# Performance work log

Measured on AMD Instinct MI355X. Metric: run time of the kernel, lower is better.

Reference implementation:

```python
import jax, jax.numpy as jnp
import numpy as np

B, S, D = 1, 2048, 2048
HQ, HKV = 32, 8
HD = D // HQ            # 64
G = HQ // HKV           # 4 query heads per kv head


def setup_inputs() -> dict:
    key = jax.random.key(0)
    ks = jax.random.split(key, 5)
    x = jax.random.normal(ks[0], (B, S, D), jnp.float32)
    # RoPE tables (theta = 10000), shape [S, HD//2]
    inv_freq = 1.0 / (10000.0 ** (np.arange(0, HD, 2, dtype=np.float64) / HD))
    angles = np.outer(np.arange(S, dtype=np.float64), inv_freq)
    freqs_cos = jnp.asarray(np.cos(angles), jnp.float32)
    freqs_sin = jnp.asarray(np.sin(angles), jnp.float32)
    # additive causal mask [1,1,S,S]: 0 on/below diagonal, large negative above
    i = jnp.arange(S)
    causal_mask = jnp.where(i[None, :] <= i[:, None], 0.0, -1e9).astype(jnp.float32)[None, None]
    sc = 1.0 / np.sqrt(D)
    Wq = jax.random.normal(ks[1], (D, HQ * HD), jnp.float32) * sc
    Wk = jax.random.normal(ks[2], (D, HKV * HD), jnp.float32) * sc
    Wv = jax.random.normal(ks[3], (D, HKV * HD), jnp.float32) * sc
    Wo = jax.random.normal(ks[4], (D, D), jnp.float32) * sc
    return {"x": x, "freqs_cos": freqs_cos, "freqs_sin": freqs_sin,
            "causal_mask": causal_mask, "Wq": Wq, "Wk": Wk, "Wv": Wv, "Wo": Wo}


def _rope(t, cos, sin):
    # t: [B,S,H,HD]; complex multiply on interleaved (even, odd) pairs
    b, s, h, d = t.shape
    t2 = t.reshape(b, s, h, d // 2, 2)
    t0, t1 = t2[..., 0], t2[..., 1]
    c = cos[None, :, None, :]
    sn = sin[None, :, None, :]
    out = jnp.stack([t0 * c - t1 * sn, t0 * sn + t1 * c], axis=-1)
    return out.reshape(b, s, h, d)


def reference(x, freqs_cos, freqs_sin, causal_mask, Wq, Wk, Wv, Wo):
    b, s, _ = x.shape
    q = (x @ Wq).reshape(b, s, HQ, HD)
    k = (x @ Wk).reshape(b, s, HKV, HD)
    v = (x @ Wv).reshape(b, s, HKV, HD)
    q = _rope(q, freqs_cos, freqs_sin)
    k = _rope(k, freqs_cos, freqs_sin)
    # GQA without materializing repeat_kv: group query heads per kv head
    q = q.transpose(0, 2, 1, 3).reshape(b, HKV, G, s, HD)   # [b,kv,g,s,d]
    k = k.transpose(0, 2, 1, 3)                              # [b,kv,s,d]
    v = v.transpose(0, 2, 1, 3)                              # [b,kv,s,d]
    scores = jnp.einsum('bkgsd,bktd->bkgst', q, k) / jnp.sqrt(jnp.float32(HD))
    scores = scores + causal_mask[:, :, None]                # [1,1,1,S,S] broadcast
    probs = jax.nn.softmax(scores, axis=-1)
    out = jnp.einsum('bkgst,bktd->bkgsd', probs, v)          # [b,kv,g,s,d]
    out = out.transpose(0, 3, 1, 2, 4).reshape(b, s, D)      # merge heads in (kv,g) order
    return out @ Wo
```

## Files before the change

### kernel.cpp

```cpp
#include <hip/hip_runtime.h>

#define SEQ 2048
#define DMODEL 2048

typedef __attribute__((ext_vector_type(8))) _Float16 half8;
typedef __attribute__((ext_vector_type(4))) float f32x4;
typedef __attribute__((ext_vector_type(16))) float f32x16;

typedef const __attribute__((address_space(1))) void* gptr_t;
typedef __attribute__((address_space(3))) void* lptr_t;

static __device__ __forceinline__ void gload16(const void* g, void* l) {
  __builtin_amdgcn_global_load_lds((gptr_t)g, (lptr_t)l, 16, 0, 0);
}

static __device__ __forceinline__ unsigned short f2h(float f) {
  _Float16 h = (_Float16)f;
  union { _Float16 h; unsigned short u; } v; v.h = h;
  return v.u;
}

static __device__ __forceinline__ unsigned int pkh2(float a, float b) {
  union { __fp16 __attribute__((ext_vector_type(2))) h; unsigned int u; } v;
  v.h = __builtin_amdgcn_cvt_pkrtz(a, b);
  return v.u;
}

__global__ void k_cvt(const float* __restrict__ in, unsigned short* __restrict__ out, int n) {
  int i = (blockIdx.x * 256 + threadIdx.x) * 4;
  if (i >= n) return;
  float4 v = *(const float4*)(in + i);
  ushort4 o;
  o.x = f2h(v.x); o.y = f2h(v.y); o.z = f2h(v.z); o.w = f2h(v.w);
  *(ushort4*)(out + i) = o;
}

__global__ void k_tcvt(const float* __restrict__ in, unsigned short* __restrict__ out,
                       int K, int N, int ldin) {
  __shared__ float tile[32][33];
  int n0 = blockIdx.x * 32, k0 = blockIdx.y * 32;
  int tx = threadIdx.x, ty = threadIdx.y;
  #pragma unroll
  for (int j = ty; j < 32; j += 8)
    tile[j][tx] = in[(long)(k0 + j) * ldin + n0 + tx];
  __syncthreads();
  #pragma unroll
  for (int j = ty; j < 32; j += 8)
    out[(long)(n0 + j) * K + k0 + tx] = f2h(tile[tx][j]);
}

__global__ void k_tvp(const unsigned short* __restrict__ in, unsigned short* __restrict__ out) {
  __shared__ unsigned short tile[32][33];
  int c0 = blockIdx.x * 32, s0 = blockIdx.y * 32;
  int tx = threadIdx.x, ty = threadIdx.y;
  #pragma unroll
  for (int j = ty; j < 32; j += 8)
    tile[j][tx] = in[(long)(s0 + j) * 512 + c0 + tx];
  __syncthreads();
  #pragma unroll
  for (int j = ty; j < 32; j += 8) {
    int c = c0 + j;
    int s = s0 + tx;
    int sp = (s & ~12) | ((s & 8) >> 1) | ((s & 4) << 1);
    out[((long)(c >> 6) * 64 + (c & 63)) * SEQ + sp] = tile[tx][j];
  }
}

static __device__ __forceinline__ void gemm_core(const unsigned short* __restrict__ A,
                                                 const unsigned short* __restrict__ B,
                                                 int K, unsigned short* As, unsigned short* Bs,
                                                 long m0, long n0, int t, int wm, int wn,
                                                 int lr, int lh, f32x4 acc[2][4]) {
  int swc = ((t & 3) ^ ((t >> 3) & 3)) * 8;
  const unsigned short* Ag = A + (m0 + (t >> 2)) * K + swc;
  const unsigned short* Bg = B + (n0 + (t >> 2)) * K + swc;
  #pragma unroll
  for (int i = 0; i < 2; i++)
    #pragma unroll
    for (int j = 0; j < 4; j++)
      acc[i][j] = (f32x4){0.f, 0.f, 0.f, 0.f};

#define STAGE(buf, k0) do { \
    gload16(Ag + (k0), As + (buf) * 4096 + t * 8); \
    gload16(Bg + (k0), Bs + (buf) * 4096 + t * 8); \
  } while (0)

  int T = K >> 5;
  STAGE(0, 0);
  STAGE(1, 32);
  asm volatile("s_waitcnt vmcnt(2)" ::: "memory");
  __builtin_amdgcn_s_barrier();

  int bi = 0;
  for (int ti = 0; ti < T; ti++) {
    if (ti + 2 < T) STAGE((bi + 2) % 3, (ti + 2) * 32);
    const unsigned short* Ab = As + bi * 4096;
    const unsigned short* Bb = Bs + bi * 4096;
    half8 a[2], b[4];
    #pragma unroll
    for (int mf = 0; mf < 2; mf++) {
      int ra = wm * 32 + mf * 16 + lr;
      a[mf] = *(const half8*)&Ab[ra * 32 + ((lh ^ ((ra >> 1) & 3)) * 8)];
    }
    #pragma unroll
    for (int nf = 0; nf < 4; nf++) {
      int rb = wn * 64 + nf * 16 + lr;
      b[nf] = *(const half8*)&Bb[rb * 32 + ((lh ^ ((rb >> 1) & 3)) * 8)];
    }
    #pragma unroll
    for (int mf = 0; mf < 2; mf++)
      #pragma unroll
      for (int nf = 0; nf < 4; nf++)
        acc[mf][nf] = __builtin_amdgcn_mfma_f32_16x16x32_f16(a[mf], b[nf], acc[mf][nf], 0, 0, 0);
    if (ti + 2 < T) asm volatile("s_waitcnt vmcnt(2)" ::: "memory");
    else            asm volatile("s_waitcnt vmcnt(0)" ::: "memory");
    __builtin_amdgcn_s_barrier();
    bi = bi == 2 ? 0 : bi + 1;
  }
#undef STAGE
}

__global__ __launch_bounds__(512) void k_gemm(const unsigned short* __restrict__ A,
                                              const unsigned short* __restrict__ B,
                                              float* __restrict__ C, int M, int N, int K) {
  __shared__ unsigned short As[3 * 4096];
  __shared__ unsigned short Bs[3 * 4096];
  int t = threadIdx.x;
  int l = t & 63, w = t >> 6;
  int wm = w >> 1, wn = w & 1;
  int lr = l & 15, lh = l >> 4;
  long m0 = (long)blockIdx.y * 128, n0 = (long)blockIdx.x * 128;
  f32x4 acc[2][4];
  gemm_core(A, B, K, As, Bs, m0, n0, t, wm, wn, lr, lh, acc);
  #pragma unroll
  for (int mf = 0; mf < 2; mf++)
    #pragma unroll
    for (int nf = 0; nf < 4; nf++)
      #pragma unroll
      for (int i = 0; i < 4; i++)
        C[(m0 + wm * 32 + mf * 16 + lh * 4 + i) * N + n0 + wn * 64 + nf * 16 + lr] = acc[mf][nf][i];
}

__global__ __launch_bounds__(512) void k_gemm_qkv(const unsigned short* __restrict__ A,
                                                  const unsigned short* __restrict__ B,
                                                  unsigned short* __restrict__ Qr,
                                                  unsigned short* __restrict__ Kr,
                                                  unsigned short* __restrict__ Vr,
                                                  const float* __restrict__ fc,
                                                  const float* __restrict__ fs, int K) {
  __shared__ unsigned short As[3 * 4096];
  __shared__ unsigned short Bs[3 * 4096];
  int t = threadIdx.x;
  int l = t & 63, w = t >> 6;
  int wm = w >> 1, wn = w & 1;
  int lr = l & 15, lh = l >> 4;
  long m0 = (long)blockIdx.y * 128, n0 = (long)blockIdx.x * 128;
  f32x4 acc[2][4];
  gemm_core(A, B, K, As, Bs, m0, n0, t, wm, wn, lr, lh, acc);

  const float SC = 0.125f * 1.44269504f;
  int n0i = (int)n0;
  if (n0i < 2560) {
    bool isQ = n0i < 2048;
    float scl = isQ ? SC : 1.0f;
    #pragma unroll
    for (int mf = 0; mf < 2; mf++)
      #pragma unroll
      for (int i = 0; i < 4; i++) {
        int row = (int)m0 + wm * 32 + mf * 16 + lh * 4 + i;
        const float* fcr = fc + row * 32;
        const float* fsr = fs + row * 32;
        #pragma unroll
        for (int nf = 0; nf < 4; nf++) {
          float v = acc[mf][nf][i];
          float pv = __shfl_xor(v, 1);
          int col = n0i + wn * 64 + nf * 16 + lr;
          int j = (col & 63) >> 1;
          float c_ = fcr[j] * scl, s_ = fsr[j] * scl;
          float o = (lr & 1) ? (pv * s_ + v * c_) : (v * c_ - pv * s_);
          if (isQ) Qr[(long)row * 2048 + col] = f2h(o);
          else {
            int cc = col - 2048;
            Kr[((long)(cc >> 6) * SEQ + row) * 64 + (cc & 63)] = f2h(o);
          }
        }
      }
  } else {
    #pragma unroll
    for (int mf = 0; mf < 2; mf++)
      #pragma unroll
      for (int i = 0; i < 4; i++) {
        int row = (int)m0 + wm * 32 + mf * 16 + lh * 4 + i;
        #pragma unroll
        for (int nf = 0; nf < 4; nf++) {
          int col = n0i + wn * 64 + nf * 16 + lr;
          Vr[(long)row * 512 + (col - 2560)] = f2h(acc[mf][nf][i]);
        }
      }
  }
}

__global__ __launch_bounds__(256) void k_attn(const unsigned short* __restrict__ Qr,
                                              const unsigned short* __restrict__ Kr,
                                              const unsigned short* __restrict__ Vg,
                                              unsigned short* __restrict__ AO) {
  __shared__ unsigned short KT[2][8192];
  __shared__ unsigned short VT[2][8192];
  __shared__ float gbuf[4][32];

  int tt = threadIdx.x;
  int wid = tt >> 6, l = tt & 63;
  int q = l & 31, hs = l >> 5;
  int h = blockIdx.x, hkv = h >> 2;
  int by = (int)gridDim.y - 1 - blockIdx.y;
  int dt = 4 * by + wid;
  int q0 = by * 128 + wid * 32;

  const unsigned short* Kh = Kr + (long)hkv * SEQ * 64;
  const unsigned short* Vh = Vg + (long)hkv * 64 * SEQ;

  int skr = tt >> 3, skc = tt & 7;
  int svr = tt >> 2, svc = tt & 3;
  const unsigned short* Ksrc = Kh + (long)skr * 64 + ((skc * 8) ^ ((skr & 7) << 3));
  const unsigned short* Vsrc = Vh + (long)svr * SEQ + ((svc * 8) ^ ((svr & 3) << 3));

#define ASTAGE(si) do { \
    int buf_ = (si) & 1; \
    _Pragma("unroll") for (int sub_ = 0; sub_ < 4; sub_++) { \
      int t0_ = ((si) * 4 + sub_) * 32; \
      gload16(Ksrc + (long)t0_ * 64, &KT[buf_][sub_ * 2048 + tt * 8]); \
      gload16(Vsrc + t0_, &VT[buf_][sub_ * 2048 + tt * 8]); \
    } \
  } while (0)

  half8 Qf[4];
  #pragma unroll
  for (int d = 0; d < 4; d++)
    Qf[d] = *(const half8*)&Qr[(long)(q0 + q) * 2048 + h * 64 + d * 16 + 8 * hs];

  f32x16 O0, O1;
  #pragma unroll
  for (int r = 0; r < 16; r++) { O0[r] = 0.f; O1[r] = 0.f; }
  float lsum = 0.f;

  ASTAGE(0);
  asm volatile("s_waitcnt vmcnt(0)" ::: "memory");
  __builtin_amdgcn_s_barrier();

  for (int si = 0; si <= by; si++) {
    if (si + 1 <= by) ASTAGE(si + 1);

    int buf = si & 1;
    #pragma unroll
    for (int sub = 0; sub < 4; sub++) {
      int ti = si * 4 + sub;
      if (ti <= dt) {
        const unsigned short* Ks = &KT[buf][sub * 2048];
        const unsigned short* Vs = &VT[buf][sub * 2048];
        half8 Kf[4], Vf[2][2];
        #pragma unroll
        for (int d = 0; d < 4; d++) {
          int e0 = d * 16 + 8 * hs;
          Kf[d] = *(const half8*)&Ks[q * 64 + (e0 ^ ((q & 7) << 3))];
        }
        #pragma unroll
        for (int ks = 0; ks < 2; ks++)
          #pragma unroll
          for (int nf = 0; nf < 2; nf++) {
            int d = q + 32 * nf;
            int e0 = ks * 16 + 8 * hs;
            Vf[ks][nf] = *(const half8*)&Vs[d * 32 + (e0 ^ ((d & 3) << 3))];
          }

        f32x16 S;
        #pragma unroll
        for (int r = 0; r < 16; r++) S[r] = 0.f;
        #pragma unroll
        for (int d = 0; d < 4; d++)
          S = __builtin_amdgcn_mfma_f32_32x32x16_f16(Kf[d], Qf[d], S, 0, 0, 0);

        bool dg = (ti == dt);
        float p[16];
        #pragma unroll
        for (int r = 0; r < 16; r++) {
          float v = S[r];
          if (dg) {
            int key = (r & 3) + 8 * (r >> 2) + 4 * hs;
            if (key > q) v = -1e30f;
          }
          p[r] = __builtin_exp2f(v - 8.0f);
          lsum += p[r];
        }

        union { unsigned int u[4]; half8 hh; } f0, f1;
        #pragma unroll
        for (int c = 0; c < 4; c++) {
          f0.u[c] = pkh2(p[2 * c], p[2 * c + 1]);
          f1.u[c] = pkh2(p[8 + 2 * c], p[9 + 2 * c]);
        }

        O0 = __builtin_amdgcn_mfma_f32_32x32x16_f16(f0.hh, Vf[0][0], O0, 0, 0, 0);
        O0 = __builtin_amdgcn_mfma_f32_32x32x16_f16(f1.hh, Vf[1][0], O0, 0, 0, 0);
        O1 = __builtin_amdgcn_mfma_f32_32x32x16_f16(f0.hh, Vf[0][1], O1, 0, 0, 0);
        O1 = __builtin_amdgcn_mfma_f32_32x32x16_f16(f1.hh, Vf[1][1], O1, 0, 0, 0);
      }
    }

    asm volatile("s_waitcnt vmcnt(0)" ::: "memory");
    __builtin_amdgcn_s_barrier();
  }
#undef ASTAGE

  lsum += __shfl_xor(lsum, 32);
  if (l < 32) gbuf[wid][l] = 1.f / lsum;
  asm volatile("" ::: "memory");
  #pragma unroll
  for (int r = 0; r < 16; r++) {
    int row = (r & 3) + 8 * (r >> 2) + 4 * hs;
    float ri = gbuf[wid][row];
    AO[(long)(q0 + row) * 2048 + h * 64 + q] = f2h(O0[r] * ri);
    AO[(long)(q0 + row) * 2048 + h * 64 + q + 32] = f2h(O1[r] * ri);
  }
}

extern "C" void kernel_launch(void* const* d_in, const int* in_sizes, int n_in,
                              void* d_out, int out_size, void* d_ws, size_t ws_size,
                              hipStream_t stream) {
  const float* x  = (const float*)d_in[0];
  const float* fc = (const float*)d_in[1];
  const float* fs = (const float*)d_in[2];
  const float* Wq = (const float*)d_in[4];
  const float* Wk = (const float*)d_in[5];
  const float* Wv = (const float*)d_in[6];
  const float* Wo = (const float*)d_in[7];
  float* out = (float*)d_out;

  char* ws = (char*)d_ws;
  unsigned short* xb  = (unsigned short*)(ws);
  unsigned short* WT  = (unsigned short*)(ws + (8l  << 20));
  unsigned short* WoT = (unsigned short*)(ws + (20l << 20));
  unsigned short* Qr  = (unsigned short*)(ws + (28l << 20));
  unsigned short* Kr  = (unsigned short*)(ws + (36l << 20));
  unsigned short* Vr  = (unsigned short*)(ws + (38l << 20));
  unsigned short* Vt  = (unsigned short*)(ws + (40l << 20));
  unsigned short* AO  = xb;

  dim3 tb(32, 8);
  k_cvt<<<4096, 256, 0, stream>>>(x, xb, 2048 * 2048);
  k_tcvt<<<dim3(64, 64), tb, 0, stream>>>(Wq, WT, 2048, 2048, 2048);
  k_tcvt<<<dim3(16, 64), tb, 0, stream>>>(Wk, WT + 2048l * 2048, 2048, 512, 512);
  k_tcvt<<<dim3(16, 64), tb, 0, stream>>>(Wv, WT + 2560l * 2048, 2048, 512, 512);
  k_tcvt<<<dim3(64, 64), tb, 0, stream>>>(Wo, WoT, 2048, 2048, 2048);

  k_gemm_qkv<<<dim3(24, 16), 512, 0, stream>>>(xb, WT, Qr, Kr, Vr, fc, fs, 2048);

  k_tvp<<<dim3(16, 64), tb, 0, stream>>>(Vr, Vt);

  k_attn<<<dim3(32, 16), 256, 0, stream>>>(Qr, Kr, Vt, AO);

  k_gemm<<<dim3(16, 16), 512, 0, stream>>>(AO, WoT, out, 2048, 2048, 2048);
}
```

Before: 172.1 us.

## Split K across warp pairs in GEMM core with LDS reduction

The shared GEMM core now uses a K-tile of 64 with double buffering instead of a K-tile of 32 with triple buffering. The 8 waves are split into two K-halves, each wave computing a 64x64 sub-tile, and the halves' partial accumulators are reduced through LDS at the end. Fewer iterations and barriers are needed, and each wave issues more MFMAs per LDS fragment load. In exchange it needs 64KB of LDS, twice the accumulator registers, an extra reduction pass, and only half the waves write results, which may reduce occupancy.

```diff
diff --git a/kernel.cpp b/kernel.cpp
--- a/kernel.cpp
+++ b/kernel.cpp
@@ -66,79 +66,104 @@
   }
 }
 
-static __device__ __forceinline__ void gemm_core(const unsigned short* __restrict__ A,
+static __device__ __forceinline__ bool gemm_core(const unsigned short* __restrict__ A,
                                                  const unsigned short* __restrict__ B,
-                                                 int K, unsigned short* As, unsigned short* Bs,
-                                                 long m0, long n0, int t, int wm, int wn,
-                                                 int lr, int lh, f32x4 acc[2][4]) {
-  int swc = ((t & 3) ^ ((t >> 3) & 3)) * 8;
-  const unsigned short* Ag = A + (m0 + (t >> 2)) * K + swc;
-  const unsigned short* Bg = B + (n0 + (t >> 2)) * K + swc;
-  #pragma unroll
-  for (int i = 0; i < 2; i++)
+                                                 int K, char* SM, long m0, long n0,
+                                                 int& wmO, int& wnO, f32x4 acc[4][4]) {
+  int t = threadIdx.x;
+  int l = t & 63, w = t >> 6;
+  int ks = w & 1, wm = (w >> 2) & 1, wn = (w >> 1) & 1;
+  int lr = l & 15, lh = l >> 4;
+  wmO = wm; wnO = wn;
+  unsigned short* As = (unsigned short*)SM;
+  unsigned short* Bs = (unsigned short*)(SM + 32768);
+
+  const unsigned short* Ag = A + (m0 + (t >> 3)) * K + (((t & 7) ^ ((t >> 3) & 7)) * 8);
+  const unsigned short* Bg = B + (n0 + (t >> 3)) * K + (((t & 7) ^ ((t >> 3) & 7)) * 8);
+
+  #pragma unroll
+  for (int i = 0; i < 4; i++)
     #pragma unroll
     for (int j = 0; j < 4; j++)
       acc[i][j] = (f32x4){0.f, 0.f, 0.f, 0.f};
 
-#define STAGE(buf, k0) do { \
-    gload16(Ag + (k0), As + (buf) * 4096 + t * 8); \
-    gload16(Bg + (k0), Bs + (buf) * 4096 + t * 8); \
+#define STG(buf, k0) do { \
+    gload16(Ag + (k0), As + (buf) * 8192 + t * 8); \
+    gload16(Ag + 64 * K + (k0), As + (buf) * 8192 + 4096 + t * 8); \
+    gload16(Bg + (k0), Bs + (buf) * 8192 + t * 8); \
+    gload16(Bg + 64 * K + (k0), Bs + (buf) * 8192 + 4096 + t * 8); \
   } while (0)
 
-  int T = K >> 5;
-  STAGE(0, 0);
-  STAGE(1, 32);
-  asm volatile("s_waitcnt vmcnt(2)" ::: "memory");
+  int T = K >> 6;
+  STG(0, 0);
+  asm volatile("s_waitcnt vmcnt(0)" ::: "memory");
   __builtin_amdgcn_s_barrier();
 
-  int bi = 0;
-  for (int ti = 0; ti < T; ti++) {
-    if (ti + 2 < T) STAGE((bi + 2) % 3, (ti + 2) * 32);
-    const unsigned short* Ab = As + bi * 4096;
-    const unsigned short* Bb = Bs + bi * 4096;
-    half8 a[2], b[4];
-    #pragma unroll
-    for (int mf = 0; mf < 2; mf++) {
-      int ra = wm * 32 + mf * 16 + lr;
-      a[mf] = *(const half8*)&Ab[ra * 32 + ((lh ^ ((ra >> 1) & 3)) * 8)];
+  for (int ph = 0; ph < T; ph++) {
+    if (ph + 1 < T) STG((ph + 1) & 1, (ph + 1) * 64);
+    const unsigned short* Ab = As + (ph & 1) * 8192;
+    const unsigned short* Bb = Bs + (ph & 1) * 8192;
+    half8 a[4], b[4];
+    #pragma unroll
+    for (int mf = 0; mf < 4; mf++) {
+      int ra = wm * 64 + mf * 16 + lr;
+      a[mf] = *(const half8*)&Ab[ra * 64 + (((ks * 4 + lh) ^ (ra & 7)) * 8)];
     }
     #pragma unroll
     for (int nf = 0; nf < 4; nf++) {
       int rb = wn * 64 + nf * 16 + lr;
-      b[nf] = *(const half8*)&Bb[rb * 32 + ((lh ^ ((rb >> 1) & 3)) * 8)];
+      b[nf] = *(const half8*)&Bb[rb * 64 + (((ks * 4 + lh) ^ (rb & 7)) * 8)];
     }
     #pragma unroll
-    for (int mf = 0; mf < 2; mf++)
+    for (int mf = 0; mf < 4; mf++)
       #pragma unroll
       for (int nf = 0; nf < 4; nf++)
         acc[mf][nf] = __builtin_amdgcn_mfma_f32_16x16x32_f16(a[mf], b[nf], acc[mf][nf], 0, 0, 0);
-    if (ti + 2 < T) asm volatile("s_waitcnt vmcnt(2)" ::: "memory");
-    else            asm volatile("s_waitcnt vmcnt(0)" ::: "memory");
+    asm volatile("s_waitcnt vmcnt(0)" ::: "memory");
     __builtin_amdgcn_s_barrier();
-    bi = bi == 2 ? 0 : bi + 1;
-  }
-#undef STAGE
+  }
+#undef STG
+
+  __syncthreads();
+  float* red = (float*)SM;
+  int p = wm * 2 + wn;
+  if (ks == 1) {
+    #pragma unroll
+    for (int mf = 0; mf < 4; mf++)
+      #pragma unroll
+      for (int nf = 0; nf < 4; nf++)
+        *(f32x4*)&red[p * 4096 + l * 64 + (((mf * 4 + nf) ^ (l & 15)) << 2)] = acc[mf][nf];
+  }
+  __syncthreads();
+  if (ks == 0) {
+    #pragma unroll
+    for (int mf = 0; mf < 4; mf++)
+      #pragma unroll
+      for (int nf = 0; nf < 4; nf++)
+        acc[mf][nf] += *(const f32x4*)&red[p * 4096 + l * 64 + (((mf * 4 + nf) ^ (l & 15)) << 2)];
+  }
+  return ks == 0;
 }
 
 __global__ __launch_bounds__(512) void k_gemm(const unsigned short* __restrict__ A,
                                               const unsigned short* __restrict__ B,
                                               float* __restrict__ C, int M, int N, int K) {
-  __shared__ unsigned short As[3 * 4096];
-  __shared__ unsigned short Bs[3 * 4096];
-  int t = threadIdx.x;
-  int l = t & 63, w = t >> 6;
-  int wm = w >> 1, wn = w & 1;
+  __shared__ __align__(16) char SM[65536];
+  int l = threadIdx.x & 63;
   int lr = l & 15, lh = l >> 4;
   long m0 = (long)blockIdx.y * 128, n0 = (long)blockIdx.x * 128;
-  f32x4 acc[2][4];
-  gemm_core(A, B, K, As, Bs, m0, n0, t, wm, wn, lr, lh, acc);
-  #pragma unroll
-  for (int mf = 0; mf < 2; mf++)
-    #pragma unroll
-    for (int nf = 0; nf < 4; nf++)
-      #pragma unroll
-      for (int i = 0; i < 4; i++)
-        C[(m0 + wm * 32 + mf * 16 + lh * 4 + i) * N + n0 + wn * 64 + nf * 16 + lr] = acc[mf][nf][i];
+  f32x4 acc[4][4];
+  int wm, wn;
+  bool own = gemm_core(A, B, K, SM, m0, n0, wm, wn, acc);
+  if (own) {
+    #pragma unroll
+    for (int mf = 0; mf < 4; mf++)
+      #pragma unroll
+      for (int nf = 0; nf < 4; nf++)
+        #pragma unroll
+        for (int i = 0; i < 4; i++)
+          C[(m0 + wm * 64 + mf * 16 + lh * 4 + i) * N + n0 + wn * 64 + nf * 16 + lr] = acc[mf][nf][i];
+  }
 }
 
 __global__ __launch_bounds__(512) void k_gemm_qkv(const unsigned short* __restrict__ A,
@@ -148,15 +173,14 @@
                                                   unsigned short* __restrict__ Vr,
                                                   const float* __restrict__ fc,
                                                   const float* __restrict__ fs, int K) {
-  __shared__ unsigned short As[3 * 4096];
-  __shared__ unsigned short Bs[3 * 4096];
-  int t = threadIdx.x;
-  int l = t & 63, w = t >> 6;
-  int wm = w >> 1, wn = w & 1;
+  __shared__ __align__(16) char SM[65536];
+  int l = threadIdx.x & 63;
   int lr = l & 15, lh = l >> 4;
   long m0 = (long)blockIdx.y * 128, n0 = (long)blockIdx.x * 128;
-  f32x4 acc[2][4];
-  gemm_core(A, B, K, As, Bs, m0, n0, t, wm, wn, lr, lh, acc);
+  f32x4 acc[4][4];
+  int wm, wn;
+  bool own = gemm_core(A, B, K, SM, m0, n0, wm, wn, acc);
+  if (!own) return;
 
   const float SC = 0.125f * 1.44269504f;
   int n0i = (int)n0;
@@ -164,10 +188,10 @@
     bool isQ = n0i < 2048;
     float scl = isQ ? SC : 1.0f;
     #pragma unroll
-    for (int mf = 0; mf < 2; mf++)
+    for (int mf = 0; mf < 4; mf++)
       #pragma unroll
       for (int i = 0; i < 4; i++) {
-        int row = (int)m0 + wm * 32 + mf * 16 + lh * 4 + i;
+        int row = (int)m0 + wm * 64 + mf * 16 + lh * 4 + i;
         const float* fcr = fc + row * 32;
         const float* fsr = fs + row * 32;
         #pragma unroll
@@ -187,10 +211,10 @@
       }
   } else {
     #pragma unroll
-    for (int mf = 0; mf < 2; mf++)
+    for (int mf = 0; mf < 4; mf++)
       #pragma unroll
       for (int i = 0; i < 4; i++) {
-        int row = (int)m0 + wm * 32 + mf * 16 + lh * 4 + i;
+        int row = (int)m0 + wm * 64 + mf * 16 + lh * 4 + i;
         #pragma unroll
         for (int nf = 0; nf < 4; nf++) {
           int col = n0i + wn * 64 + nf * 16 + lr;
```

Result: faster. 156.9 us (-8.8%).
